# Performance work log

Hardware: AMD Instinct MI355X
Metric: run time of the kernel (lower is better)

## Reference

```python
import jax, jax.numpy as jnp
import numpy as np
import math

B, S, HID, H = 2, 4096, 512, 8
D_K = HID // H


def setup_inputs() -> dict:
    key = jax.random.key(0)
    ks = jax.random.split(key, 8)
    inp = {
        "query": jax.random.normal(ks[0], (B, S, HID), dtype=jnp.float32),
        "key": jax.random.normal(ks[1], (B, S, HID), dtype=jnp.float32),
        "value": jax.random.normal(ks[2], (B, S, HID), dtype=jnp.float32),
        "mask": jax.random.randint(ks[3], (B, S), 0, 2, dtype=jnp.int32),
        # conv1d kernel_size=1, bias=False -> plain [out,in] weights (xavier-normal-ish)
        "Wq": jax.random.normal(ks[4], (HID, HID), dtype=jnp.float32) * (1.0 / math.sqrt(HID)),
        "Wk": jax.random.normal(ks[5], (HID, HID), dtype=jnp.float32) * (1.0 / math.sqrt(HID)),
        "Wv": jax.random.normal(ks[6], (HID, HID), dtype=jnp.float32) * (1.0 / math.sqrt(HID)),
        "Wo": jax.random.normal(ks[7], (HID, HID), dtype=jnp.float32) * (1.0 / math.sqrt(HID)),
    }
    return inp


def reference(query, key, value, mask, Wq, Wk, Wv, Wo):
    b, s, _ = query.shape
    # conv1d(k=1, bias=False) projection == x @ W.T; split heads -> [b,h,s,d_k]
    def proj(x, W):
        return jnp.einsum('bsd,ed->bse', x, W).reshape(b, s, H, D_K).transpose(0, 2, 1, 3)
    q, k, v = proj(query, Wq), proj(key, Wk), proj(value, Wv)
    # NOTE: original scales by 1/log(d_k), not 1/sqrt(d_k)
    score = jnp.einsum('bhqd,bhkd->bhqk', q, k) / math.log(D_K)
    m = mask.reshape(b, 1, 1, s)  # broadcast over heads and query positions
    score = jnp.where(m == 0, jnp.float32(-1e30), score)
    attn = jax.nn.softmax(score, axis=-1)  # dropout is identity in eval
    x = jnp.einsum('bhqk,bhkd->bhqd', attn, v)
    x = x.transpose(0, 2, 1, 3).reshape(b, s, HID)
    return jnp.einsum('bsd,ed->bse', x, Wo)
```

## Files before the change

### kernel.cpp

```cpp
#include <hip/hip_runtime.h>
#include <hip/hip_bf16.h>
#include <cstdint>
#include <cstddef>


namespace {

constexpr int kB = 2, kS = 4096, kHid = 512, kH = 8, kDk = 64;
constexpr int kBH = kB * kH;
constexpr int kM = kB * kS;

typedef __attribute__((ext_vector_type(8))) short short8;
typedef __attribute__((ext_vector_type(2))) float float2v;
typedef __attribute__((ext_vector_type(4))) float floatx4;
typedef __attribute__((ext_vector_type(16))) float floatx16;
typedef __attribute__((ext_vector_type(4))) unsigned int uintx4;
typedef unsigned short u16;

__device__ __forceinline__ u16 bf16rne(float f) {
    uint32_t u = __float_as_uint(f);
    u += 0x7fffu + ((u >> 16) & 1u);
    return (u16)(u >> 16);
}
__device__ __forceinline__ uint32_t pk2(float lo, float hi) {
#if __has_builtin(__builtin_amdgcn_cvt_pk_bf16_f32)
    typedef __attribute__((ext_vector_type(2))) __bf16 bf2;
    bf2 h = __builtin_amdgcn_cvt_pk_bf16_f32(lo, hi);
    return __builtin_bit_cast(uint32_t, h);
#else
    return ((uint32_t)bf16rne(hi) << 16) | (uint32_t)bf16rne(lo);
#endif
}
__device__ __forceinline__ float fexp2(float x) {
#if __has_builtin(__builtin_amdgcn_exp2f)
    return __builtin_amdgcn_exp2f(x);
#else
    return exp2f(x);
#endif
}
__device__ __forceinline__ float bf2f(u16 v) {
    return __uint_as_float((uint32_t)v << 16);
}
__device__ __forceinline__ void plswap(uint32_t& a, uint32_t& b) {
#if __has_builtin(__builtin_amdgcn_permlane32_swap)
    typedef __attribute__((ext_vector_type(2))) unsigned int uint2v;
    uint2v r = __builtin_amdgcn_permlane32_swap(a, b, false, false);
    a = r[0]; b = r[1];
#else
    asm volatile("v_permlane32_swap_b32 %0, %1" : "+v"(a), "+v"(b));
#endif
}
__device__ __forceinline__ void gload16(const void* g, void* l) {
    __builtin_amdgcn_global_load_lds(
        (const __attribute__((address_space(1))) void*)g,
        (__attribute__((address_space(3))) void*)l, 16, 0, 0);
}

__global__ __launch_bounds__(256) void cvt_qw(const float* __restrict__ q,
    const float* __restrict__ k, const float* __restrict__ v,
    const float* __restrict__ w0, const float* __restrict__ w1,
    const float* __restrict__ w2, const float* __restrict__ w3,
    u16* __restrict__ xall, u16* __restrict__ wall) {
    const int bx = blockIdx.x;
    if (bx < 12288) {
        int z = bx >> 12;
        size_t i = (size_t)(bx & 4095) * 256 + threadIdx.x;
        const float* src = z == 0 ? q : (z == 1 ? k : v);
        float4 f = ((const float4*)src)[i];
        ushort4 o;
        o.x = bf16rne(f.x); o.y = bf16rne(f.y);
        o.z = bf16rne(f.z); o.w = bf16rne(f.w);
        ((ushort4*)(xall + (size_t)z * kM * kHid))[i] = o;
    } else {
        int r = bx - 12288;
        int z = r >> 8;
        size_t i = (size_t)(r & 255) * 256 + threadIdx.x;
        const float* src = z == 0 ? w0 : (z == 1 ? w1 : (z == 2 ? w2 : w3));
        float sc = (z == 0)
            ? (float)(1.4426950408889634 / (6.0 * 0.6931471805599453))
            : 1.0f;
        float4 f = ((const float4*)src)[i];
        ushort4 o;
        o.x = bf16rne(f.x * sc); o.y = bf16rne(f.y * sc);
        o.z = bf16rne(f.z * sc); o.w = bf16rne(f.w * sc);
        ((ushort4*)(wall + (size_t)z * kHid * kHid))[i] = o;
    }
}

__global__ __launch_bounds__(256) void cvt_mask(const int* __restrict__ mask,
    float* __restrict__ fb) {
    int i = blockIdx.x * 256 + threadIdx.x;
    fb[i] = mask[i] ? 0.0f : -1e30f;
}

__global__ __launch_bounds__(256, 3) void proj(const u16* __restrict__ xall,
    const u16* __restrict__ wall, u16* __restrict__ qp, u16* __restrict__ kp,
    u16* __restrict__ vt) {
    __shared__ float smt[4][16][68];
    const int z = blockIdx.z;
    const u16* x = xall + (size_t)z * kM * kHid;
    const u16* w = wall + (size_t)z * kHid * kHid;
    const int wv = threadIdx.x >> 6, lane = threadIdx.x & 63;
    const int quad = lane >> 4, l16 = lane & 15;
    const int mb = blockIdx.y * 128 + (wv >> 1) * 64;
    const int nb = blockIdx.x * 128 + (wv & 1) * 64;
    floatx4 acc[4][4] = {};
    const u16* xr = x + (size_t)(mb + l16) * kHid + quad * 8;
    const u16* wr = w + (size_t)(nb + l16) * kHid + quad * 8;
    for (int k0 = 0; k0 < kHid; k0 += 32) {
        short8 a[4], bt[4];
#pragma unroll
        for (int i = 0; i < 4; i++)
            a[i] = *(const short8*)(xr + (size_t)i * 16 * kHid + k0);
#pragma unroll
        for (int t = 0; t < 4; t++)
            bt[t] = *(const short8*)(wr + (size_t)t * 16 * kHid + k0);
        if (z == 2) {
#pragma unroll
            for (int i = 0; i < 4; i++)
#pragma unroll
            for (int t = 0; t < 4; t++)
                acc[i][t] = __builtin_amdgcn_mfma_f32_16x16x32_bf16(bt[t], a[i], acc[i][t], 0, 0, 0);
        } else {
#pragma unroll
            for (int i = 0; i < 4; i++)
#pragma unroll
            for (int t = 0; t < 4; t++)
                acc[i][t] = __builtin_amdgcn_mfma_f32_16x16x32_bf16(a[i], bt[t], acc[i][t], 0, 0, 0);
        }
    }
    if (z < 2) {
        u16* dst = (z == 0) ? qp : kp;
        const int row16 = lane >> 2, cseg = (lane & 3) * 16;
#pragma unroll
        for (int i = 0; i < 4; i++) {
#pragma unroll
            for (int t = 0; t < 4; t++)
#pragma unroll
            for (int r = 0; r < 4; r++)
                smt[wv][quad * 4 + r][t * 16 + l16] = acc[i][t][r];
            __builtin_amdgcn_wave_barrier();
            const float* rp = &smt[wv][row16][cseg];
            float4 f0 = *(const float4*)(rp);
            float4 f1 = *(const float4*)(rp + 4);
            float4 f2 = *(const float4*)(rp + 8);
            float4 f3 = *(const float4*)(rp + 12);
            uint4 o0, o1;
            o0.x = pk2(f0.x, f0.y); o0.y = pk2(f0.z, f0.w);
            o0.z = pk2(f1.x, f1.y); o0.w = pk2(f1.z, f1.w);
            o1.x = pk2(f2.x, f2.y); o1.y = pk2(f2.z, f2.w);
            o1.z = pk2(f3.x, f3.y); o1.w = pk2(f3.z, f3.w);
            u16* dp = dst + (size_t)(mb + i * 16 + row16) * kHid + nb + cseg;
            *(uint4*)dp = o0;
            *(uint4*)(dp + 8) = o1;
            __builtin_amdgcn_wave_barrier();
        }
    } else {
        const int b = mb >> 12, s0 = mb & (kS - 1);
        const int row16 = lane >> 2, cseg = (lane & 3) * 16;
#pragma unroll
        for (int t = 0; t < 4; t++) {
#pragma unroll
            for (int i = 0; i < 4; i++)
#pragma unroll
            for (int r = 0; r < 4; r++)
                smt[wv][quad * 4 + r][i * 16 + l16] = acc[i][t][r];
            __builtin_amdgcn_wave_barrier();
            const float* rp = &smt[wv][row16][cseg];
            float4 f0 = *(const float4*)(rp);
            float4 f1 = *(const float4*)(rp + 4);
            float4 f2 = *(const float4*)(rp + 8);
            float4 f3 = *(const float4*)(rp + 12);
            uint4 o0, o1;
            o0.x = pk2(f0.x, f0.y); o0.y = pk2(f0.z, f0.w);
            o0.z = pk2(f1.x, f1.y); o0.w = pk2(f1.z, f1.w);
            o1.x = pk2(f2.x, f2.y); o1.y = pk2(f2.z, f2.w);
            o1.z = pk2(f3.x, f3.y); o1.w = pk2(f3.z, f3.w);
            const int n = nb + t * 16 + row16;
            const int h = n >> 6, d = n & (kDk - 1);
            u16* dp = vt + ((size_t)(b * kH + h) * kDk + d) * kS + s0 + cseg;
            *(uint4*)dp = o0;
            *(uint4*)(dp + 8) = o1;
            __builtin_amdgcn_wave_barrier();
        }
    }
}

__global__ __launch_bounds__(256, 2) void attn(const u16* __restrict__ qp,
    const u16* __restrict__ kp, const u16* __restrict__ vt,
    const float* __restrict__ fbias, u16* __restrict__ ows,
    float* __restrict__ rsws) {
    union SmT {
        struct { u16 K[3][64][64]; u16 V[3][64][64]; float B[3][256]; } s;
        float ep[4][32][33];
    };
    __shared__ __align__(16) SmT sm;
    const int tid = threadIdx.x;
    const int wv = tid >> 6, l = tid & 63;
    const int hf = l >> 5, q32 = l & 31, l7 = l & 7;
    const int wg = blockIdx.x;
    const int bh = ((wg & 7) << 1) | ((wg >> 3) & 1);
    const int qb = (wg >> 4) & 15;
    const int kz = wg >> 8;
    const int b = bh >> 3, h = bh & 7;
    const int qbase = qb * 256 + wv * 64;
    const u16* Qb = qp + (size_t)b * kS * kHid + h * 64;
    const u16* Kb = kp + (size_t)b * kS * kHid + h * 64;
    const u16* Vb = vt + (size_t)bh * kDk * kS;
    const float* fm = fbias + b * kS;

    short8 qf[2][4];
#pragma unroll
    for (int qt = 0; qt < 2; qt++)
#pragma unroll
    for (int m = 0; m < 4; m++)
        qf[qt][m] = *(const short8*)(Qb + (size_t)(qbase + qt * 32 + q32) * kHid + m * 16 + hf * 8);

    floatx16 O[2][2] = {};
    float rs[2] = {0.0f, 0.0f};

    const int srow = l >> 3;
    const int pcol = (l7 ^ srow) * 8;
    const u16* pK = Kb + (size_t)(kz * 64 + wv * 8 + srow) * kHid + pcol;
    const u16* pV = Vb + (size_t)(wv * 8 + srow) * kS + kz * 64 + pcol;
    const float* pB = fm + kz * 64 + (l & 15) * 4;
    auto stage = [&](int buf) {
        gload16(pK,                     &sm.s.K[buf][wv * 8][0]);
        gload16(pK + (size_t)32 * kHid, &sm.s.K[buf][wv * 8 + 32][0]);
        gload16(pV,                     &sm.s.V[buf][wv * 8][0]);
        gload16(pV + (size_t)32 * kS,   &sm.s.V[buf][wv * 8 + 32][0]);
        gload16(pB,                     &sm.s.B[buf][0]);
        pK += (size_t)128 * kHid;
        pV += 128;
        pB += 128;
    };

    auto compute = [&](int buf) {
#pragma unroll
        for (int ks = 0; ks < 2; ++ks) {
            short8 kf[4];
#pragma unroll
            for (int m = 0; m < 4; m++)
                kf[m] = *(const short8*)&sm.s.K[buf][ks * 32 + q32][((2 * m + hf) ^ l7) * 8];
            short8 vf[2][2];
#pragma unroll
            for (int ds = 0; ds < 2; ds++)
#pragma unroll
            for (int tt = 0; tt < 2; tt++)
                vf[ds][tt] = *(const short8*)&sm.s.V[buf][ds * 32 + q32][((ks * 4 + tt * 2 + hf) ^ l7) * 8];
            const float* bb = &sm.s.B[buf][ks * 32 + 4 * hf];
            float4 g0 = *(const float4*)(bb);
            float4 g1 = *(const float4*)(bb + 8);
            float4 g2 = *(const float4*)(bb + 16);
            float4 g3 = *(const float4*)(bb + 24);
#pragma unroll
            for (int qt = 0; qt < 2; ++qt) {
                floatx16 st;
                st[0] = g0.x;  st[1] = g0.y;  st[2] = g0.z;  st[3] = g0.w;
                st[4] = g1.x;  st[5] = g1.y;  st[6] = g1.z;  st[7] = g1.w;
                st[8] = g2.x;  st[9] = g2.y;  st[10] = g2.z; st[11] = g2.w;
                st[12] = g3.x; st[13] = g3.y; st[14] = g3.z; st[15] = g3.w;
#pragma unroll
                for (int m = 0; m < 4; m++)
                    st = __builtin_amdgcn_mfma_f32_32x32x16_bf16(kf[m], qf[qt][m], st, 0, 0, 0);
                float xx[16];
#pragma unroll
                for (int r = 0; r < 16; r++) xx[r] = fexp2(st[r]);
                float2v a0 = {xx[0], xx[1]},  a1 = {xx[2], xx[3]};
                float2v a2 = {xx[4], xx[5]},  a3 = {xx[6], xx[7]};
                float2v a4 = {xx[8], xx[9]},  a5 = {xx[10], xx[11]};
                float2v a6 = {xx[12], xx[13]}, a7 = {xx[14], xx[15]};
                a0 += a1; a2 += a3; a4 += a5; a6 += a7;
                a0 += a2; a4 += a6;
                a0 += a4;
                rs[qt] += a0[0] + a0[1];
                uint32_t w00 = pk2(xx[0], xx[1]),   w01 = pk2(xx[2], xx[3]);
                uint32_t w10 = pk2(xx[4], xx[5]),   w11 = pk2(xx[6], xx[7]);
                uint32_t w20 = pk2(xx[8], xx[9]),   w21 = pk2(xx[10], xx[11]);
                uint32_t w30 = pk2(xx[12], xx[13]), w31 = pk2(xx[14], xx[15]);
                plswap(w00, w10); plswap(w01, w11);
                plswap(w20, w30); plswap(w21, w31);
                uintx4 t0 = {w00, w01, w10, w11};
                uintx4 t1 = {w20, w21, w30, w31};
                short8 bf0 = __builtin_bit_cast(short8, t0);
                short8 bf1 = __builtin_bit_cast(short8, t1);
                O[qt][0] = __builtin_amdgcn_mfma_f32_32x32x16_bf16(vf[0][0], bf0, O[qt][0], 0, 0, 0);
                O[qt][0] = __builtin_amdgcn_mfma_f32_32x32x16_bf16(vf[0][1], bf1, O[qt][0], 0, 0, 0);
                O[qt][1] = __builtin_amdgcn_mfma_f32_32x32x16_bf16(vf[1][0], bf0, O[qt][1], 0, 0, 0);
                O[qt][1] = __builtin_amdgcn_mfma_f32_32x32x16_bf16(vf[1][1], bf1, O[qt][1], 0, 0, 0);
            }
        }
    };

    stage(0);
    stage(1);
    for (int t = 0; t < 30; ++t) {
        asm volatile("s_waitcnt vmcnt(5)" ::: "memory");
        __builtin_amdgcn_s_barrier();
        __builtin_amdgcn_sched_barrier(0);
        stage((t + 2) % 3);
        compute(t % 3);
    }
    asm volatile("s_waitcnt vmcnt(5)" ::: "memory");
    __builtin_amdgcn_s_barrier();
    __builtin_amdgcn_sched_barrier(0);
    compute(0);
    asm volatile("s_waitcnt vmcnt(0)" ::: "memory");
    __builtin_amdgcn_s_barrier();
    __builtin_amdgcn_sched_barrier(0);
    compute(1);
    __syncthreads();

#pragma unroll
    for (int qt = 0; qt < 2; ++qt) {
        float r = rs[qt];
        r += __shfl_xor(r, 32);
        if (hf == 0)
            rsws[((size_t)kz * kBH + bh) * kS + qbase + qt * 32 + q32] = r;
        u16* Ob = ows + (((size_t)kz * kBH + bh) * kS + qbase + qt * 32) * kDk;
#pragma unroll
        for (int ds = 0; ds < 2; ds++) {
#pragma unroll
            for (int rr = 0; rr < 16; rr++)
                sm.ep[wv][q32][(rr & 3) + 8 * (rr >> 2) + 4 * hf] = O[qt][ds][rr];
            __builtin_amdgcn_wave_barrier();
            {
                const int qq = l >> 1, c0 = (l & 1) * 16;
                float f[16];
#pragma unroll
                for (int j = 0; j < 16; j++) f[j] = sm.ep[wv][qq][c0 + j];
                uint4 o0, o1;
                o0.x = pk2(f[0], f[1]);   o0.y = pk2(f[2], f[3]);
                o0.z = pk2(f[4], f[5]);   o0.w = pk2(f[6], f[7]);
                o1.x = pk2(f[8], f[9]);   o1.y = pk2(f[10], f[11]);
                o1.z = pk2(f[12], f[13]); o1.w = pk2(f[14], f[15]);
                u16* dp = Ob + (size_t)qq * kDk + ds * 32 + c0;
                *(uint4*)dp = o0;
                *(uint4*)(dp + 8) = o1;
            }
            __builtin_amdgcn_wave_barrier();
        }
    }
}

__global__ __launch_bounds__(256) void combine(const u16* __restrict__ ows,
    const float* __restrict__ rsws, u16* __restrict__ xo) {
    size_t i = (size_t)blockIdx.x * 256 + threadIdx.x;
    const int d8 = (int)(i & 7);
    const int s  = (int)((i >> 3) & (kS - 1));
    const int bh = (int)(i >> 15);
    const int b = bh >> 3, h = bh & 7;
    const size_t base = ((size_t)bh * kS + s) * kDk + d8 * 8;
    short8 a = *(const short8*)(ows + base);
    short8 c = *(const short8*)(ows + (size_t)kBH * kS * kDk + base);
    float r = rsws[(size_t)bh * kS + s] + rsws[(size_t)kBH * kS + (size_t)bh * kS + s];
    float inv = 1.0f / r;
    float e[8];
#pragma unroll
    for (int j = 0; j < 8; j++)
        e[j] = (bf2f((u16)a[j]) + bf2f((u16)c[j])) * inv;
    uint4 o;
    o.x = pk2(e[0], e[1]); o.y = pk2(e[2], e[3]);
    o.z = pk2(e[4], e[5]); o.w = pk2(e[6], e[7]);
    *(uint4*)(xo + ((size_t)b * kS + s) * kHid + h * 64 + d8 * 8) = o;
}

__global__ __launch_bounds__(256, 3) void oproj(const u16* __restrict__ x,
    const u16* __restrict__ w, float* __restrict__ out) {
    const int wv = threadIdx.x >> 6, lane = threadIdx.x & 63;
    const int quad = lane >> 4, l16 = lane & 15;
    const int mb = blockIdx.y * 128 + (wv >> 1) * 64;
    const int nb = blockIdx.x * 128 + (wv & 1) * 64;
    floatx4 acc[4][4] = {};
    const u16* xr = x + (size_t)(mb + l16) * kHid + quad * 8;
    const u16* wr = w + (size_t)(nb + l16) * kHid + quad * 8;
    for (int k0 = 0; k0 < kHid; k0 += 32) {
        short8 a[4], bt[4];
#pragma unroll
        for (int i = 0; i < 4; i++)
            a[i] = *(const short8*)(xr + (size_t)i * 16 * kHid + k0);
#pragma unroll
        for (int t = 0; t < 4; t++)
            bt[t] = *(const short8*)(wr + (size_t)t * 16 * kHid + k0);
#pragma unroll
        for (int i = 0; i < 4; i++)
#pragma unroll
        for (int t = 0; t < 4; t++)
            acc[i][t] = __builtin_amdgcn_mfma_f32_16x16x32_bf16(a[i], bt[t], acc[i][t], 0, 0, 0);
    }
#pragma unroll
    for (int i = 0; i < 4; i++)
#pragma unroll
    for (int t = 0; t < 4; t++)
#pragma unroll
    for (int r = 0; r < 4; r++) {
        int m = mb + i * 16 + quad * 4 + r;
        int n = nb + t * 16 + l16;
        out[(size_t)m * kHid + n] = acc[i][t][r];
    }
}

}

extern "C" void kernel_launch(void* const* d_in, const int* in_sizes, int n_in,
                              void* d_out, int out_size, void* d_ws, size_t ws_size,
                              hipStream_t stream) {
    const float* q  = (const float*)d_in[0];
    const float* k  = (const float*)d_in[1];
    const float* v  = (const float*)d_in[2];
    const int* mask = (const int*)d_in[3];
    const float* w0 = (const float*)d_in[4];
    const float* w1 = (const float*)d_in[5];
    const float* w2 = (const float*)d_in[6];
    const float* w3 = (const float*)d_in[7];
    float* out = (float*)d_out;

    u16* ws   = (u16*)d_ws;
    u16* xall = ws;
    u16* wall = xall + (size_t)3 * kM * kHid;
    u16* qp   = wall + (size_t)4 * kHid * kHid;
    u16* kp   = qp + (size_t)kBH * kS * kDk;
    u16* vt   = kp + (size_t)kBH * kS * kDk;
    u16* ows  = xall;
    float* fbias = (float*)wall;
    float* rsws  = fbias + (size_t)kB * kS;
    u16* xo   = qp;

    dim3 blk(256);
    cvt_qw <<<dim3(13312), blk, 0, stream>>>(q, k, v, w0, w1, w2, w3, xall, wall);
    proj   <<<dim3(kHid / 128, kM / 128, 3), blk, 0, stream>>>(xall, wall, qp, kp, vt);
    cvt_mask<<<dim3(kB * kS / 256), blk, 0, stream>>>(mask, fbias);
    attn   <<<dim3(512), blk, 0, stream>>>(qp, kp, vt, fbias, ows, rsws);
    combine<<<dim3(2048), blk, 0, stream>>>(ows, rsws, xo);
    oproj  <<<dim3(kHid / 128, kM / 128), blk, 0, stream>>>(
        xo, wall + (size_t)3 * kHid * kHid, out);
}
```

Measured before the change: 263.7 us.

## Stage projection GEMM tiles through double-buffered swizzled LDS with async loads

Rewrites the proj and oproj GEMM main loops so that 128x64 A and B tiles are loaded into double-buffered LDS with direct global-to-LDS loads (gload16), using an XOR swizzle to avoid bank conflicts. Each wave then reads its MFMA fragments from LDS instead of issuing scattered per-wave global loads, so the block shares the tile data and the next tile's load overlaps the current compute. This costs 64KB of LDS per block, and the occupancy hint is lowered from 3 to 2 blocks to match.

```diff
diff --git a/kernel.cpp b/kernel.cpp
--- a/kernel.cpp
+++ b/kernel.cpp
@@ -93,42 +93,79 @@
     fb[i] = mask[i] ? 0.0f : -1e30f;
 }
 
-__global__ __launch_bounds__(256, 3) void proj(const u16* __restrict__ xall,
+__global__ __launch_bounds__(256, 2) void proj(const u16* __restrict__ xall,
     const u16* __restrict__ wall, u16* __restrict__ qp, u16* __restrict__ kp,
     u16* __restrict__ vt) {
-    __shared__ float smt[4][16][68];
+    union PS {
+        struct { u16 A[2][128][64]; u16 B[2][128][64]; } s;
+        float smt[4][16][68];
+    };
+    __shared__ __align__(16) PS sm;
     const int z = blockIdx.z;
     const u16* x = xall + (size_t)z * kM * kHid;
     const u16* w = wall + (size_t)z * kHid * kHid;
-    const int wv = threadIdx.x >> 6, lane = threadIdx.x & 63;
+    const int tid = threadIdx.x;
+    const int wv = tid >> 6, lane = tid & 63;
     const int quad = lane >> 4, l16 = lane & 15;
-    const int mb = blockIdx.y * 128 + (wv >> 1) * 64;
-    const int nb = blockIdx.x * 128 + (wv & 1) * 64;
+    const int mb = blockIdx.y * 128, nb = blockIdx.x * 128;
+    const int mw = (wv >> 1) * 64, nw = (wv & 1) * 64;
     floatx4 acc[4][4] = {};
-    const u16* xr = x + (size_t)(mb + l16) * kHid + quad * 8;
-    const u16* wr = w + (size_t)(nb + l16) * kHid + quad * 8;
-    for (int k0 = 0; k0 < kHid; k0 += 32) {
-        short8 a[4], bt[4];
-#pragma unroll
-        for (int i = 0; i < 4; i++)
-            a[i] = *(const short8*)(xr + (size_t)i * 16 * kHid + k0);
-#pragma unroll
-        for (int t = 0; t < 4; t++)
-            bt[t] = *(const short8*)(wr + (size_t)t * 16 * kHid + k0);
-        if (z == 2) {
+
+    const int srow = lane >> 3, sch = lane & 7;
+    const int scol = (sch ^ srow) * 8;
+    const u16* pA = x + (size_t)(mb + wv * 8 + srow) * kHid + scol;
+    const u16* pB = w + (size_t)(nb + wv * 8 + srow) * kHid + scol;
+    auto stage = [&](int buf) {
+#pragma unroll
+        for (int j = 0; j < 4; j++) {
+            gload16(pA + (size_t)(j * 32) * kHid, &sm.s.A[buf][j * 32 + wv * 8][0]);
+            gload16(pB + (size_t)(j * 32) * kHid, &sm.s.B[buf][j * 32 + wv * 8][0]);
+        }
+        pA += 64; pB += 64;
+    };
+    auto compute = [&](int buf) {
+#pragma unroll
+        for (int hh = 0; hh < 2; hh++) {
+            short8 a[4], bt[4];
 #pragma unroll
             for (int i = 0; i < 4; i++)
+                a[i] = *(const short8*)&sm.s.A[buf][mw + i * 16 + l16]
+                        [(((hh << 2) | quad) ^ (l16 & 7)) * 8];
 #pragma unroll
             for (int t = 0; t < 4; t++)
-                acc[i][t] = __builtin_amdgcn_mfma_f32_16x16x32_bf16(bt[t], a[i], acc[i][t], 0, 0, 0);
-        } else {
-#pragma unroll
-            for (int i = 0; i < 4; i++)
-#pragma unroll
-            for (int t = 0; t < 4; t++)
-                acc[i][t] = __builtin_amdgcn_mfma_f32_16x16x32_bf16(a[i], bt[t], acc[i][t], 0, 0, 0);
-        }
-    }
+                bt[t] = *(const short8*)&sm.s.B[buf][nw + t * 16 + l16]
+                        [(((hh << 2) | quad) ^ (l16 & 7)) * 8];
+            if (z == 2) {
+#pragma unroll
+                for (int i = 0; i < 4; i++)
+#pragma unroll
+                for (int t = 0; t < 4; t++)
+                    acc[i][t] = __builtin_amdgcn_mfma_f32_16x16x32_bf16(bt[t], a[i], acc[i][t], 0, 0, 0);
+            } else {
+#pragma unroll
+                for (int i = 0; i < 4; i++)
+#pragma unroll
+                for (int t = 0; t < 4; t++)
+                    acc[i][t] = __builtin_amdgcn_mfma_f32_16x16x32_bf16(a[i], bt[t], acc[i][t], 0, 0, 0);
+            }
+        }
+    };
+
+    stage(0);
+    asm volatile("s_waitcnt vmcnt(0)" ::: "memory");
+    __builtin_amdgcn_s_barrier();
+    int buf = 0;
+    for (int t = 0; t < 7; ++t) {
+        stage(buf ^ 1);
+        compute(buf);
+        asm volatile("s_waitcnt vmcnt(0)" ::: "memory");
+        __builtin_amdgcn_s_barrier();
+        buf ^= 1;
+    }
+    compute(buf);
+    __syncthreads();
+
+    const int mbw = mb + mw, nbw = nb + nw;
     if (z < 2) {
         u16* dst = (z == 0) ? qp : kp;
         const int row16 = lane >> 2, cseg = (lane & 3) * 16;
@@ -138,9 +175,9 @@
             for (int t = 0; t < 4; t++)
 #pragma unroll
             for (int r = 0; r < 4; r++)
-                smt[wv][quad * 4 + r][t * 16 + l16] = acc[i][t][r];
+                sm.smt[wv][quad * 4 + r][t * 16 + l16] = acc[i][t][r];
             __builtin_amdgcn_wave_barrier();
-            const float* rp = &smt[wv][row16][cseg];
+            const float* rp = &sm.smt[wv][row16][cseg];
             float4 f0 = *(const float4*)(rp);
             float4 f1 = *(const float4*)(rp + 4);
             float4 f2 = *(const float4*)(rp + 8);
@@ -150,13 +187,13 @@
             o0.z = pk2(f1.x, f1.y); o0.w = pk2(f1.z, f1.w);
             o1.x = pk2(f2.x, f2.y); o1.y = pk2(f2.z, f2.w);
             o1.z = pk2(f3.x, f3.y); o1.w = pk2(f3.z, f3.w);
-            u16* dp = dst + (size_t)(mb + i * 16 + row16) * kHid + nb + cseg;
+            u16* dp = dst + (size_t)(mbw + i * 16 + row16) * kHid + nbw + cseg;
             *(uint4*)dp = o0;
             *(uint4*)(dp + 8) = o1;
             __builtin_amdgcn_wave_barrier();
         }
     } else {
-        const int b = mb >> 12, s0 = mb & (kS - 1);
+        const int b = mbw >> 12, s0 = mbw & (kS - 1);
         const int row16 = lane >> 2, cseg = (lane & 3) * 16;
 #pragma unroll
         for (int t = 0; t < 4; t++) {
@@ -164,9 +201,9 @@
             for (int i = 0; i < 4; i++)
 #pragma unroll
             for (int r = 0; r < 4; r++)
-                smt[wv][quad * 4 + r][i * 16 + l16] = acc[i][t][r];
+                sm.smt[wv][quad * 4 + r][i * 16 + l16] = acc[i][t][r];
             __builtin_amdgcn_wave_barrier();
-            const float* rp = &smt[wv][row16][cseg];
+            const float* rp = &sm.smt[wv][row16][cseg];
             float4 f0 = *(const float4*)(rp);
             float4 f1 = *(const float4*)(rp + 4);
             float4 f2 = *(const float4*)(rp + 8);
@@ -176,7 +213,7 @@
             o0.z = pk2(f1.x, f1.y); o0.w = pk2(f1.z, f1.w);
             o1.x = pk2(f2.x, f2.y); o1.y = pk2(f2.z, f2.w);
             o1.z = pk2(f3.x, f3.y); o1.w = pk2(f3.z, f3.w);
-            const int n = nb + t * 16 + row16;
+            const int n = nbw + t * 16 + row16;
             const int h = n >> 6, d = n & (kDk - 1);
             u16* dp = vt + ((size_t)(b * kH + h) * kDk + d) * kS + s0 + cseg;
             *(uint4*)dp = o0;
@@ -365,37 +402,70 @@
     *(uint4*)(xo + ((size_t)b * kS + s) * kHid + h * 64 + d8 * 8) = o;
 }
 
-__global__ __launch_bounds__(256, 3) void oproj(const u16* __restrict__ x,
+__global__ __launch_bounds__(256, 2) void oproj(const u16* __restrict__ x,
     const u16* __restrict__ w, float* __restrict__ out) {
-    const int wv = threadIdx.x >> 6, lane = threadIdx.x & 63;
+    __shared__ __align__(16) u16 A[2][128][64];
+    __shared__ __align__(16) u16 Bt[2][128][64];
+    const int tid = threadIdx.x;
+    const int wv = tid >> 6, lane = tid & 63;
     const int quad = lane >> 4, l16 = lane & 15;
-    const int mb = blockIdx.y * 128 + (wv >> 1) * 64;
-    const int nb = blockIdx.x * 128 + (wv & 1) * 64;
+    const int mb = blockIdx.y * 128, nb = blockIdx.x * 128;
+    const int mw = (wv >> 1) * 64, nw = (wv & 1) * 64;
     floatx4 acc[4][4] = {};
-    const u16* xr = x + (size_t)(mb + l16) * kHid + quad * 8;
-    const u16* wr = w + (size_t)(nb + l16) * kHid + quad * 8;
-    for (int k0 = 0; k0 < kHid; k0 += 32) {
-        short8 a[4], bt[4];
-#pragma unroll
-        for (int i = 0; i < 4; i++)
-            a[i] = *(const short8*)(xr + (size_t)i * 16 * kHid + k0);
-#pragma unroll
-        for (int t = 0; t < 4; t++)
-            bt[t] = *(const short8*)(wr + (size_t)t * 16 * kHid + k0);
-#pragma unroll
-        for (int i = 0; i < 4; i++)
-#pragma unroll
-        for (int t = 0; t < 4; t++)
-            acc[i][t] = __builtin_amdgcn_mfma_f32_16x16x32_bf16(a[i], bt[t], acc[i][t], 0, 0, 0);
-    }
+    const int srow = lane >> 3, sch = lane & 7;
+    const int scol = (sch ^ srow) * 8;
+    const u16* pA = x + (size_t)(mb + wv * 8 + srow) * kHid + scol;
+    const u16* pB = w + (size_t)(nb + wv * 8 + srow) * kHid + scol;
+    auto stage = [&](int buf) {
+#pragma unroll
+        for (int j = 0; j < 4; j++) {
+            gload16(pA + (size_t)(j * 32) * kHid, &A[buf][j * 32 + wv * 8][0]);
+            gload16(pB + (size_t)(j * 32) * kHid, &Bt[buf][j * 32 + wv * 8][0]);
+        }
+        pA += 64; pB += 64;
+    };
+    auto compute = [&](int buf) {
+#pragma unroll
+        for (int hh = 0; hh < 2; hh++) {
+            short8 a[4], bt[4];
+#pragma unroll
+            for (int i = 0; i < 4; i++)
+                a[i] = *(const short8*)&A[buf][mw + i * 16 + l16]
+                        [(((hh << 2) | quad) ^ (l16 & 7)) * 8];
+#pragma unroll
+            for (int t = 0; t < 4; t++)
+                bt[t] = *(const short8*)&Bt[buf][nw + t * 16 + l16]
+                        [(((hh << 2) | quad) ^ (l16 & 7)) * 8];
+#pragma unroll
+            for (int i = 0; i < 4; i++)
+#pragma unroll
+            for (int t = 0; t < 4; t++)
+                acc[i][t] = __builtin_amdgcn_mfma_f32_16x16x32_bf16(a[i], bt[t], acc[i][t], 0, 0, 0);
+        }
+    };
+
+    stage(0);
+    asm volatile("s_waitcnt vmcnt(0)" ::: "memory");
+    __builtin_amdgcn_s_barrier();
+    int buf = 0;
+    for (int t = 0; t < 7; ++t) {
+        stage(buf ^ 1);
+        compute(buf);
+        asm volatile("s_waitcnt vmcnt(0)" ::: "memory");
+        __builtin_amdgcn_s_barrier();
+        buf ^= 1;
+    }
+    compute(buf);
+
+    const int mbw = mb + mw, nbw = nb + nw;
 #pragma unroll
     for (int i = 0; i < 4; i++)
 #pragma unroll
     for (int t = 0; t < 4; t++)
 #pragma unroll
     for (int r = 0; r < 4; r++) {
-        int m = mb + i * 16 + quad * 4 + r;
-        int n = nb + t * 16 + l16;
+        int m = mbw + i * 16 + quad * 4 + r;
+        int n = nbw + t * 16 + l16;
         out[(size_t)m * kHid + n] = acc[i][t][r];
     }
 }
```

New measurement: 234.0 us. 11.3% less time.
